# Optimization experiments

Hardware: AMD Instinct MI355X
Metric: run time of the kernel (lower is better)

## Reference

```python
import jax, jax.numpy as jnp
import numpy as np

B, N, FDIM, REL, H = 4, 256, 256, 16, 8
D = FDIM // H


def setup_inputs() -> dict:
    key = jax.random.key(0)
    ks = jax.random.split(key, 10)
    s_f = 1.0 / np.sqrt(FDIM)
    s_kv = 1.0 / np.sqrt(FDIM + REL)
    return {
        "node_features": jax.random.normal(ks[0], (B, N, FDIM), jnp.float32),
        "relative_positions": jax.random.normal(ks[1], (B, N, N, REL), jnp.float32),
        # torch Linear weights stored transposed -> here [in, out]
        "Wq": jax.random.uniform(ks[2], (FDIM, FDIM), jnp.float32, -s_f, s_f),
        "bq": jax.random.uniform(ks[3], (FDIM,), jnp.float32, -s_f, s_f),
        "Wk": jax.random.uniform(ks[4], (FDIM + REL, FDIM), jnp.float32, -s_kv, s_kv),
        "bk": jax.random.uniform(ks[5], (FDIM,), jnp.float32, -s_kv, s_kv),
        "Wv": jax.random.uniform(ks[6], (FDIM + REL, FDIM), jnp.float32, -s_kv, s_kv),
        "bv": jax.random.uniform(ks[7], (FDIM,), jnp.float32, -s_kv, s_kv),
        "Wo": jax.random.uniform(ks[8], (FDIM, FDIM), jnp.float32, -s_f, s_f),
        "bo": jax.random.uniform(ks[9], (FDIM,), jnp.float32, -s_f, s_f),
    }


def reference(node_features, relative_positions, Wq, bq, Wk, bk, Wv, bv, Wo, bo):
    b, n, f = node_features.shape
    # Q: [b, n_i, H, D]
    Q = (node_features @ Wq + bq).reshape(b, n, H, D)
    # per-edge K/V input: [b, i, j, f+rel] where feature part is node j's features
    nf_j = jnp.broadcast_to(node_features[:, None, :, :], (b, n, n, f))
    kv_in = jnp.concatenate([nf_j, relative_positions], axis=-1)
    K = (kv_in @ Wk + bk).reshape(b, n, n, H, D)  # [b, i, j, h, d]
    V = (kv_in @ Wv + bv).reshape(b, n, n, H, D)
    scale = 1.0 / jnp.sqrt(jnp.asarray(D, node_features.dtype))
    scores = jnp.einsum('bihd,bijhd->bhij', Q, K) * scale
    attn = jax.nn.softmax(scores, axis=-1)
    wv = jnp.einsum('bhij,bijhd->bihd', attn, V).reshape(b, n, f)
    return node_features + (wv @ Wo + bo)
```

## Files before the change

### kernel.cpp

```cpp
#include <hip/hip_runtime.h>


#define BB 4
#define NN 256
#define FD 256
#define RL 16
#define NH 8
#define HD 32

#define OFF_Q    0
#define OFF_KN   (BB*NN*FD)
#define OFF_VN   (OFF_KN + BB*NN*FD/2)
#define OFF_WO   (OFF_VN + BB*NN*FD/2)

#define ATP 260
#define RLT 262

static __device__ __forceinline__ unsigned short f2bf(float x) {
  unsigned int u = __float_as_uint(x);
  unsigned int r = (u + 0x7fffu + ((u >> 16) & 1u)) >> 16;
  return (unsigned short)r;
}
static __device__ __forceinline__ float bf2f(unsigned short h) {
  return __uint_as_float(((unsigned int)h) << 16);
}

__global__ __launch_bounds__(512) void k_qkv6(
    const float* __restrict__ nf,
    const float* __restrict__ Wq, const float* __restrict__ bq,
    const float* __restrict__ Wk, const float* __restrict__ bk,
    const float* __restrict__ Wv, const float* __restrict__ bv,
    const float* __restrict__ Wo,
    float* __restrict__ ws) {
  const int tid = threadIdx.x;
  const int sel = blockIdx.y;
  if (sel == 3) {
    if (tid < 256) {
      const int k2 = blockIdx.x;
      unsigned int lo = f2bf(Wo[(2 * k2) * FD + tid]);
      unsigned int hi = f2bf(Wo[(2 * k2 + 1) * FD + tid]);
      ((unsigned int*)(ws + OFF_WO))[k2 * FD + tid] = lo | (hi << 16);
    }
    return;
  }
  __shared__ __align__(16) float lrowT[FD * 12];
  const int row0 = blockIdx.x * 8;
  const float* W; const float* bias;
  if (sel == 0)      { W = Wq; bias = bq; }
  else if (sel == 1) { W = Wk; bias = bk; }
  else               { W = Wv; bias = bv; }
  #pragma unroll
  for (int t = 0; t < 4; ++t) {
    int idx = tid + t * 512;
    int k = idx & 255, r = idx >> 8;
    lrowT[k * 12 + r] = nf[(row0 + r) * FD + k];
  }
  __syncthreads();
  const int col = tid & 255, half = tid >> 8;
  float acc[8];
  #pragma unroll
  for (int r = 0; r < 8; ++r) acc[r] = 0.f;
  {
    const float* Wp = W + (half * 128) * FD + col;
    const float* lp = lrowT + (half * 128) * 12;
    #pragma unroll 8
    for (int kk = 0; kk < 128; ++kk) {
      const float w = Wp[kk * FD];
      float4 a0 = *(const float4*)&lp[kk * 12];
      float4 a1 = *(const float4*)&lp[kk * 12 + 4];
      acc[0] += a0.x * w; acc[1] += a0.y * w; acc[2] += a0.z * w; acc[3] += a0.w * w;
      acc[4] += a1.x * w; acc[5] += a1.y * w; acc[6] += a1.z * w; acc[7] += a1.w * w;
    }
  }
  __syncthreads();
  float* red = lrowT;
  if (half) {
    #pragma unroll
    for (int r = 0; r < 8; ++r) red[r * 256 + col] = acc[r];
  }
  __syncthreads();
  if (!half) {
    #pragma unroll
    for (int r = 0; r < 8; ++r) acc[r] += red[r * 256 + col];
    const float bb = bias[col];
    if (sel == 1) {
      const int b2 = row0 >> 8, i0 = row0 & 255;
      unsigned short* kout = (unsigned short*)(ws + OFF_KN) + ((size_t)b2 * FD + col) * NN + i0;
      ushort4 v0, v1;
      v0.x = f2bf(acc[0] + bb); v0.y = f2bf(acc[1] + bb);
      v0.z = f2bf(acc[2] + bb); v0.w = f2bf(acc[3] + bb);
      v1.x = f2bf(acc[4] + bb); v1.y = f2bf(acc[5] + bb);
      v1.z = f2bf(acc[6] + bb); v1.w = f2bf(acc[7] + bb);
      ((ushort4*)kout)[0] = v0;
      ((ushort4*)kout)[1] = v1;
    } else if (sel == 2) {
      unsigned short* outp = (unsigned short*)(ws + OFF_VN);
      #pragma unroll
      for (int r = 0; r < 8; ++r)
        outp[(size_t)(row0 + r) * FD + col] = f2bf(acc[r] + bb);
    } else {
      float* outp = ws + OFF_Q;
      #pragma unroll
      for (int r = 0; r < 8; ++r)
        outp[(row0 + r) * FD + col] = acc[r] + bb;
    }
  }
}

__global__ __launch_bounds__(512, 1) void k_attn6(
    const float* __restrict__ rel,
    const float* __restrict__ Wk,
    const float* __restrict__ Wv,
    const float* __restrict__ nf,
    const float* __restrict__ bo,
    float* __restrict__ out,
    float* __restrict__ ws) {
  const float* Q = ws + OFF_Q;
  const unsigned short* KnB = (const unsigned short*)(ws + OFF_KN);
  const unsigned short* VnB = (const unsigned short*)(ws + OFF_VN);
  const unsigned int* WoP = (const unsigned int*)(ws + OFF_WO);

  const int bid = (blockIdx.x & 7) * 64 + (blockIdx.x >> 3);
  const int b  = bid >> 7;
  const int i0 = (bid & 127) * 2;
  const int tid = threadIdx.x;
  const int l = tid & 63, w = tid >> 6;

  __shared__ float q[2][FD];
  __shared__ float qrs[2][NH * RL];
  __shared__ __align__(16) float rldsT[2 * RL * RLT];
  __shared__ float at[2 * NH * ATP];
  __shared__ float ar[2][NH * RL];
  float* part = rldsT;
  float* wvT  = rldsT + 16 * 256;

  const float scale = 0.17677669529663687f;
  q[tid >> 8][tid & 255] = Q[(b * NN + i0 + (tid >> 8)) * FD + (tid & 255)] * scale;

  {
    const int ii = w >> 2, q4 = w & 3;
    const float4* rp = (const float4*)(rel + ((size_t)(b * NN + i0 + ii)) * (NN * RL));
    #pragma unroll
    for (int m = 0; m < 4; ++m) {
      const int j = l + 64 * m;
      float4 v = rp[j * 4 + q4];
      rldsT[(ii * RL + 4 * q4 + 0) * RLT + j] = v.x;
      rldsT[(ii * RL + 4 * q4 + 1) * RLT + j] = v.y;
      rldsT[(ii * RL + 4 * q4 + 2) * RLT + j] = v.z;
      rldsT[(ii * RL + 4 * q4 + 3) * RLT + j] = v.w;
    }
  }
  __syncthreads();

  if (tid < 256) {
    const int ii = tid >> 7, h = (tid >> 4) & 7, r = tid & 15;
    const float* wrow = Wk + (FD + r) * FD + h * HD;
    const float* qq = &q[ii][h * HD];
    float a = 0.f;
    #pragma unroll
    for (int d = 0; d < HD; ++d) a += qq[d] * wrow[d];
    qrs[ii][h * RL + r] = a;
  }

  float s[2][4] = {{0.f,0.f,0.f,0.f},{0.f,0.f,0.f,0.f}};
  {
    const ushort2* krow = (const ushort2*)(KnB + ((size_t)b * FD + w * HD) * NN);
    const float* q0 = &q[0][w * HD];
    const float* q1 = &q[1][w * HD];
    #pragma unroll 4
    for (int d = 0; d < HD; ++d) {
      ushort2 ua = krow[d * 128 + l];
      ushort2 ub = krow[d * 128 + 64 + l];
      float k0 = bf2f(ua.x), k1 = bf2f(ua.y), k2 = bf2f(ub.x), k3 = bf2f(ub.y);
      float qa = q0[d], qb = q1[d];
      s[0][0] += qa * k0; s[0][1] += qa * k1; s[0][2] += qa * k2; s[0][3] += qa * k3;
      s[1][0] += qb * k0; s[1][1] += qb * k1; s[1][2] += qb * k2; s[1][3] += qb * k3;
    }
  }
  __syncthreads();

  #pragma unroll
  for (int ii = 0; ii < 2; ++ii) {
    #pragma unroll
    for (int r = 0; r < RL; ++r) {
      const float qv = qrs[ii][w * RL + r];
      const float* rr = &rldsT[(ii * RL + r) * RLT];
      float2 ra = *(const float2*)&rr[2 * l];
      float2 rb = *(const float2*)&rr[2 * l + 128];
      s[ii][0] += qv * ra.x; s[ii][1] += qv * ra.y;
      s[ii][2] += qv * rb.x; s[ii][3] += qv * rb.y;
    }
  }

  #pragma unroll
  for (int ii = 0; ii < 2; ++ii) {
    float v = fmaxf(fmaxf(s[ii][0], s[ii][1]), fmaxf(s[ii][2], s[ii][3]));
    #pragma unroll
    for (int off = 32; off; off >>= 1) v = fmaxf(v, __shfl_xor(v, off));
    float p0 = __expf(s[ii][0] - v), p1 = __expf(s[ii][1] - v);
    float p2 = __expf(s[ii][2] - v), p3 = __expf(s[ii][3] - v);
    float sum = p0 + p1 + p2 + p3;
    #pragma unroll
    for (int off = 32; off; off >>= 1) sum += __shfl_xor(sum, off);
    const float rec = 1.f / sum;
    *(float2*)&at[(ii * NH + w) * ATP + 2 * l]       = make_float2(p0 * rec, p1 * rec);
    *(float2*)&at[(ii * NH + w) * ATP + 2 * l + 128] = make_float2(p2 * rec, p3 * rec);
  }

  #pragma unroll
  for (int ii = 0; ii < 2; ++ii) {
    const int r = l & 15, q4 = l >> 4;
    const float* arow = &at[(ii * NH + w) * ATP];
    const float* rrow = &rldsT[(ii * RL + r) * RLT];
    float a = 0.f;
    #pragma unroll 4
    for (int jj = 0; jj < 64; ++jj) {
      const int j = 4 * jj + q4;
      a += arow[j] * rrow[j];
    }
    a += __shfl_xor(a, 16);
    a += __shfl_xor(a, 32);
    if (l < 16) ar[ii][w * RL + l] = a;
  }
  __syncthreads();

  {
    const int h = l >> 4;
    const ushort2* vrow = (const ushort2*)(VnB + (size_t)b * NN * FD);
    float a00=0.f,a01=0.f,a02=0.f,a03=0.f, a10=0.f,a11=0.f,a12=0.f,a13=0.f;
    #pragma unroll 4
    for (int jj = 0; jj < 32; ++jj) {
      const int j = 32 * w + jj;
      ushort2 ua = vrow[j * 128 + l];
      ushort2 ub = vrow[j * 128 + 64 + l];
      float v0 = bf2f(ua.x), v1 = bf2f(ua.y), v2 = bf2f(ub.x), v3 = bf2f(ub.y);
      float p0  = at[h * ATP + j];
      float p0b = at[(h + 4) * ATP + j];
      float p1  = at[(NH + h) * ATP + j];
      float p1b = at[(NH + h + 4) * ATP + j];
      a00 += p0 * v0;  a01 += p0 * v1;  a02 += p0b * v2; a03 += p0b * v3;
      a10 += p1 * v0;  a11 += p1 * v1;  a12 += p1b * v2; a13 += p1b * v3;
    }
    *(float2*)&part[(0 * NH + w) * 256 + 2 * l]       = make_float2(a00, a01);
    *(float2*)&part[(0 * NH + w) * 256 + 2 * l + 128] = make_float2(a02, a03);
    *(float2*)&part[(1 * NH + w) * 256 + 2 * l]       = make_float2(a10, a11);
    *(float2*)&part[(1 * NH + w) * 256 + 2 * l + 128] = make_float2(a12, a13);
  }
  __syncthreads();

  {
    const int ii = tid >> 8, c = tid & 255, h2 = c >> 5;
    float sE = 0.f;
    #pragma unroll
    for (int w2 = 0; w2 < 8; ++w2) sE += part[(ii * NH + w2) * 256 + c];
    #pragma unroll
    for (int r = 0; r < RL; ++r)
      sE += ar[ii][h2 * RL + r] * Wv[(FD + r) * FD + c];
    wvT[c * 2 + ii] = sE;
  }
  __syncthreads();

  {
    const int ii = tid >> 8, c = tid & 255;
    float acc = 0.f;
    #pragma unroll 8
    for (int k2 = 0; k2 < 128; ++k2) {
      unsigned int u = WoP[k2 * FD + c];
      float w0 = bf2f((unsigned short)(u & 0xffffu));
      float w1 = bf2f((unsigned short)(u >> 16));
      acc += wvT[(2 * k2) * 2 + ii] * w0 + wvT[(2 * k2 + 1) * 2 + ii] * w1;
    }
    const int row = b * NN + i0 + ii;
    out[row * FD + c] = nf[row * FD + c] + acc + bo[c];
  }
}

extern "C" void kernel_launch(void* const* d_in, const int* in_sizes, int n_in,
                              void* d_out, int out_size, void* d_ws, size_t ws_size,
                              hipStream_t stream) {
  const float* nf  = (const float*)d_in[0];
  const float* rel = (const float*)d_in[1];
  const float* Wq  = (const float*)d_in[2];
  const float* bq  = (const float*)d_in[3];
  const float* Wk  = (const float*)d_in[4];
  const float* bk  = (const float*)d_in[5];
  const float* Wv  = (const float*)d_in[6];
  const float* bv  = (const float*)d_in[7];
  const float* Wo  = (const float*)d_in[8];
  const float* bo  = (const float*)d_in[9];
  float* out = (float*)d_out;
  float* ws  = (float*)d_ws;

  k_qkv6 <<<dim3(BB * NN / 8, 4), 512, 0, stream>>>(nf, Wq, bq, Wk, bk, Wv, bv, Wo, ws);
  k_attn6<<<BB * NN / 2, 512, 0, stream>>>(rel, Wk, Wv, nf, bo, out, ws);
}
```

Measured before the change: 43.00 us.

## Fuse QKV projection into attention kernel with grid-wide atomic barrier

```diff
diff --git a/kernel.cpp b/kernel.cpp
--- a/kernel.cpp
+++ b/kernel.cpp
@@ -7,11 +7,12 @@
 #define RL 16
 #define NH 8
 #define HD 32
-
-#define OFF_Q    0
-#define OFF_KN   (BB*NN*FD)
-#define OFF_VN   (OFF_KN + BB*NN*FD/2)
+#define NBLK 512
+
+#define OFF_KN   0
+#define OFF_VN   (BB*NN*FD/2)
 #define OFF_WO   (OFF_VN + BB*NN*FD/2)
+#define OFF_SYNC (OFF_WO + FD*FD/2)
 
 #define ATP 260
 #define RLT 262
@@ -25,100 +26,17 @@
   return __uint_as_float(((unsigned int)h) << 16);
 }
 
-__global__ __launch_bounds__(512) void k_qkv6(
-    const float* __restrict__ nf,
+__global__ __launch_bounds__(512, 4) void k_fused(
+    const float* __restrict__ nf, const float* __restrict__ rel,
     const float* __restrict__ Wq, const float* __restrict__ bq,
     const float* __restrict__ Wk, const float* __restrict__ bk,
     const float* __restrict__ Wv, const float* __restrict__ bv,
-    const float* __restrict__ Wo,
-    float* __restrict__ ws) {
-  const int tid = threadIdx.x;
-  const int sel = blockIdx.y;
-  if (sel == 3) {
-    if (tid < 256) {
-      const int k2 = blockIdx.x;
-      unsigned int lo = f2bf(Wo[(2 * k2) * FD + tid]);
-      unsigned int hi = f2bf(Wo[(2 * k2 + 1) * FD + tid]);
-      ((unsigned int*)(ws + OFF_WO))[k2 * FD + tid] = lo | (hi << 16);
-    }
-    return;
-  }
-  __shared__ __align__(16) float lrowT[FD * 12];
-  const int row0 = blockIdx.x * 8;
-  const float* W; const float* bias;
-  if (sel == 0)      { W = Wq; bias = bq; }
-  else if (sel == 1) { W = Wk; bias = bk; }
-  else               { W = Wv; bias = bv; }
-  #pragma unroll
-  for (int t = 0; t < 4; ++t) {
-    int idx = tid + t * 512;
-    int k = idx & 255, r = idx >> 8;
-    lrowT[k * 12 + r] = nf[(row0 + r) * FD + k];
-  }
-  __syncthreads();
-  const int col = tid & 255, half = tid >> 8;
-  float acc[8];
-  #pragma unroll
-  for (int r = 0; r < 8; ++r) acc[r] = 0.f;
-  {
-    const float* Wp = W + (half * 128) * FD + col;
-    const float* lp = lrowT + (half * 128) * 12;
-    #pragma unroll 8
-    for (int kk = 0; kk < 128; ++kk) {
-      const float w = Wp[kk * FD];
-      float4 a0 = *(const float4*)&lp[kk * 12];
-      float4 a1 = *(const float4*)&lp[kk * 12 + 4];
-      acc[0] += a0.x * w; acc[1] += a0.y * w; acc[2] += a0.z * w; acc[3] += a0.w * w;
-      acc[4] += a1.x * w; acc[5] += a1.y * w; acc[6] += a1.z * w; acc[7] += a1.w * w;
-    }
-  }
-  __syncthreads();
-  float* red = lrowT;
-  if (half) {
-    #pragma unroll
-    for (int r = 0; r < 8; ++r) red[r * 256 + col] = acc[r];
-  }
-  __syncthreads();
-  if (!half) {
-    #pragma unroll
-    for (int r = 0; r < 8; ++r) acc[r] += red[r * 256 + col];
-    const float bb = bias[col];
-    if (sel == 1) {
-      const int b2 = row0 >> 8, i0 = row0 & 255;
-      unsigned short* kout = (unsigned short*)(ws + OFF_KN) + ((size_t)b2 * FD + col) * NN + i0;
-      ushort4 v0, v1;
-      v0.x = f2bf(acc[0] + bb); v0.y = f2bf(acc[1] + bb);
-      v0.z = f2bf(acc[2] + bb); v0.w = f2bf(acc[3] + bb);
-      v1.x = f2bf(acc[4] + bb); v1.y = f2bf(acc[5] + bb);
-      v1.z = f2bf(acc[6] + bb); v1.w = f2bf(acc[7] + bb);
-      ((ushort4*)kout)[0] = v0;
-      ((ushort4*)kout)[1] = v1;
-    } else if (sel == 2) {
-      unsigned short* outp = (unsigned short*)(ws + OFF_VN);
-      #pragma unroll
-      for (int r = 0; r < 8; ++r)
-        outp[(size_t)(row0 + r) * FD + col] = f2bf(acc[r] + bb);
-    } else {
-      float* outp = ws + OFF_Q;
-      #pragma unroll
-      for (int r = 0; r < 8; ++r)
-        outp[(row0 + r) * FD + col] = acc[r] + bb;
-    }
-  }
-}
-
-__global__ __launch_bounds__(512, 1) void k_attn6(
-    const float* __restrict__ rel,
-    const float* __restrict__ Wk,
-    const float* __restrict__ Wv,
-    const float* __restrict__ nf,
-    const float* __restrict__ bo,
-    float* __restrict__ out,
-    float* __restrict__ ws) {
-  const float* Q = ws + OFF_Q;
+    const float* __restrict__ Wo, const float* __restrict__ bo,
+    float* __restrict__ out, float* __restrict__ ws) {
   const unsigned short* KnB = (const unsigned short*)(ws + OFF_KN);
   const unsigned short* VnB = (const unsigned short*)(ws + OFF_VN);
   const unsigned int* WoP = (const unsigned int*)(ws + OFF_WO);
+  unsigned int* syncp = (unsigned int*)(ws + OFF_SYNC);
 
   const int bid = (blockIdx.x & 7) * 64 + (blockIdx.x >> 3);
   const int b  = bid >> 7;
@@ -126,17 +44,77 @@
   const int tid = threadIdx.x;
   const int l = tid & 63, w = tid >> 6;
 
+  __shared__ float nfT[FD][2];
   __shared__ float q[2][FD];
   __shared__ float qrs[2][NH * RL];
   __shared__ __align__(16) float rldsT[2 * RL * RLT];
-  __shared__ float at[2 * NH * ATP];
+  __shared__ __align__(16) float at[2 * NH * ATP];
   __shared__ float ar[2][NH * RL];
+  float* red  = at;
   float* part = rldsT;
   float* wvT  = rldsT + 16 * 256;
 
-  const float scale = 0.17677669529663687f;
-  q[tid >> 8][tid & 255] = Q[(b * NN + i0 + (tid >> 8)) * FD + (tid & 255)] * scale;
-
+  {
+    const int r0 = tid >> 8, k0 = tid & 255;
+    nfT[k0][r0] = nf[(b * NN + i0 + r0) * FD + k0];
+  }
+  __syncthreads();
+  const int col = tid & 255, half = tid >> 8;
+  float aq0=0.f,aq1=0.f,ak0=0.f,ak1=0.f,av0=0.f,av1=0.f;
+  {
+    const float* wqp = Wq + (half * 128) * FD + col;
+    const float* wkp = Wk + (half * 128) * FD + col;
+    const float* wvp = Wv + (half * 128) * FD + col;
+    const float* np  = &nfT[half * 128][0];
+    #pragma unroll 8
+    for (int kk = 0; kk < 128; ++kk) {
+      float2 nv = *(const float2*)&np[kk * 2];
+      float wq_ = wqp[kk * FD], wk_ = wkp[kk * FD], wv_ = wvp[kk * FD];
+      aq0 += nv.x * wq_; aq1 += nv.y * wq_;
+      ak0 += nv.x * wk_; ak1 += nv.y * wk_;
+      av0 += nv.x * wv_; av1 += nv.y * wv_;
+    }
+  }
+  __syncthreads();
+  if (half) {
+    red[0*256+col]=aq0; red[1*256+col]=aq1;
+    red[2*256+col]=ak0; red[3*256+col]=ak1;
+    red[4*256+col]=av0; red[5*256+col]=av1;
+  }
+  __syncthreads();
+  if (!half) {
+    const float scale = 0.17677669529663687f;
+    aq0 += red[0*256+col]; aq1 += red[1*256+col];
+    ak0 += red[2*256+col]; ak1 += red[3*256+col];
+    av0 += red[4*256+col]; av1 += red[5*256+col];
+    q[0][col] = (aq0 + bq[col]) * scale;
+    q[1][col] = (aq1 + bq[col]) * scale;
+    const float bkc = bk[col];
+    unsigned int kp = (unsigned int)f2bf(ak0 + bkc)
+                    | ((unsigned int)f2bf(ak1 + bkc) << 16);
+    ((unsigned int*)(ws + OFF_KN))[((size_t)b * FD + col) * (NN/2) + (i0 >> 1)] = kp;
+    const float bvc = bv[col];
+    unsigned short* vp = (unsigned short*)(ws + OFF_VN);
+    vp[((size_t)b * NN + i0)     * FD + col] = f2bf(av0 + bvc);
+    vp[((size_t)b * NN + i0 + 1) * FD + col] = f2bf(av1 + bvc);
+  }
+  if (blockIdx.x < 128 && tid < 256) {
+    const int k2 = blockIdx.x;
+    unsigned int lo = f2bf(Wo[(2 * k2) * FD + tid]);
+    unsigned int hi = f2bf(Wo[(2 * k2 + 1) * FD + tid]);
+    ((unsigned int*)(ws + OFF_WO))[k2 * FD + tid] = lo | (hi << 16);
+  }
+  __syncthreads();
+
+  if (tid < 256) {
+    const int ii = tid >> 7, h = (tid >> 4) & 7, r = tid & 15;
+    const float* wrow = Wk + (FD + r) * FD + h * HD;
+    const float* qq = &q[ii][h * HD];
+    float a = 0.f;
+    #pragma unroll
+    for (int d = 0; d < HD; ++d) a += qq[d] * wrow[d];
+    qrs[ii][h * RL + r] = a;
+  }
   {
     const int ii = w >> 2, q4 = w & 3;
     const float4* rp = (const float4*)(rel + ((size_t)(b * NN + i0 + ii)) * (NN * RL));
@@ -150,17 +128,17 @@
       rldsT[(ii * RL + 4 * q4 + 3) * RLT + j] = v.w;
     }
   }
-  __syncthreads();
-
-  if (tid < 256) {
-    const int ii = tid >> 7, h = (tid >> 4) & 7, r = tid & 15;
-    const float* wrow = Wk + (FD + r) * FD + h * HD;
-    const float* qq = &q[ii][h * HD];
-    float a = 0.f;
-    #pragma unroll
-    for (int d = 0; d < HD; ++d) a += qq[d] * wrow[d];
-    qrs[ii][h * RL + r] = a;
-  }
+
+  __syncthreads();
+  if (tid == 0) {
+    __threadfence();
+    __hip_atomic_fetch_add(syncp, 1u, __ATOMIC_ACQ_REL, __HIP_MEMORY_SCOPE_AGENT);
+    while (__hip_atomic_load(syncp, __ATOMIC_ACQUIRE, __HIP_MEMORY_SCOPE_AGENT) < NBLK) {
+      __builtin_amdgcn_s_sleep(2);
+    }
+    __threadfence();
+  }
+  __syncthreads();
 
   float s[2][4] = {{0.f,0.f,0.f,0.f},{0.f,0.f,0.f,0.f}};
   {
@@ -177,8 +155,6 @@
       s[1][0] += qb * k0; s[1][1] += qb * k1; s[1][2] += qb * k2; s[1][3] += qb * k3;
     }
   }
-  __syncthreads();
-
   #pragma unroll
   for (int ii = 0; ii < 2; ++ii) {
     #pragma unroll
@@ -191,7 +167,6 @@
       s[ii][2] += qv * rb.x; s[ii][3] += qv * rb.y;
     }
   }
-
   #pragma unroll
   for (int ii = 0; ii < 2; ++ii) {
     float v = fmaxf(fmaxf(s[ii][0], s[ii][1]), fmaxf(s[ii][2], s[ii][3]));
@@ -206,7 +181,6 @@
     *(float2*)&at[(ii * NH + w) * ATP + 2 * l]       = make_float2(p0 * rec, p1 * rec);
     *(float2*)&at[(ii * NH + w) * ATP + 2 * l + 128] = make_float2(p2 * rec, p3 * rec);
   }
-
   #pragma unroll
   for (int ii = 0; ii < 2; ++ii) {
     const int r = l & 15, q4 = l >> 4;
@@ -271,7 +245,7 @@
       acc += wvT[(2 * k2) * 2 + ii] * w0 + wvT[(2 * k2 + 1) * 2 + ii] * w1;
     }
     const int row = b * NN + i0 + ii;
-    out[row * FD + c] = nf[row * FD + c] + acc + bo[c];
+    out[row * FD + c] = nfT[c][ii] + acc + bo[c];
   }
 }
 
@@ -291,6 +265,6 @@
   float* out = (float*)d_out;
   float* ws  = (float*)d_ws;
 
-  k_qkv6 <<<dim3(BB * NN / 8, 4), 512, 0, stream>>>(nf, Wq, bq, Wk, bk, Wv, bv, Wo, ws);
-  k_attn6<<<BB * NN / 2, 512, 0, stream>>>(rel, Wk, Wv, nf, bo, out, ws);
-}
+  hipMemsetAsync((char*)d_ws + (size_t)OFF_SYNC * 4, 0, 64, stream);
+  k_fused<<<NBLK, 512, 0, stream>>>(nf, rel, Wq, bq, Wk, bk, Wv, bv, Wo, bo, out, ws);
+}
```

Measured after the change: 129.3 us. 201% more time.
